# Performance work log

Measured on AMD Instinct MI355X. Metric: run time of the kernel, lower is better.

## Reference

```python
import jax, jax.numpy as jnp
import numpy as np

# int64 needed: hash primes (2654435761) exceed int32 range, matching torch int64 math
jax.config.update("jax_enable_x64", True)

T = 524288          # hash table size
F = 2               # features per entry
D = 3               # spatial dim
RES_MIN, RES_MAX, L, LAYER = 16.0, 512.0, 16, 8
GROWTH = np.exp((np.log(RES_MAX) - np.log(RES_MIN)) / (L - 1))
RES = float(GROWTH ** LAYER * RES_MIN)
PRIMES = jnp.array([1, 2654435761, 805459861], dtype=jnp.int64)
N_POINTS = 2097152  # I*R*M

# corner c uses ceil on dim d iff bit (D-1-d) of c is set, matching the torch corner ordering
_CORNER_MASK = ((jnp.arange(8)[:, None] >> (2 - jnp.arange(3)[None, :])) & 1).astype(bool)  # (8,3)


def setup_inputs() -> dict:
    key = jax.random.key(0)
    k1, k2 = jax.random.split(key)
    X = jax.random.uniform(k1, (N_POINTS, D), dtype=jnp.float32)
    hash_table = jax.random.normal(k2, (T, F), dtype=jnp.float32) * 1e-4
    return {"X": X, "hash_table": hash_table}


def reference(X, hash_table):
    Xs = X * (RES - 1.0)                      # (N,3)
    fl = jnp.floor(Xs)
    ce = jnp.ceil(Xs)
    fli = fl.astype(jnp.int64)
    cei = ce.astype(jnp.int64)
    # (N,8,3) cube corner integer coords
    cube = jnp.where(_CORNER_MASK[None], cei[:, None, :], fli[:, None, :])
    hm = cube * PRIMES                        # (N,8,3)
    idx = jnp.remainder(hm[..., 0] ^ hm[..., 1] ^ hm[..., 2], T)  # (N,8)
    vals = hash_table[idx]                    # (N,8,F) gather
    # trilinear interpolation, corner ordering as in the torch code
    w = Xs - fl                               # (N,3)
    w0, w1, w2 = w[:, 0:1], w[:, 1:2], w[:, 2:3]
    p00 = vals[:, 0] * (1 - w0) + vals[:, 4] * w0
    p01 = vals[:, 1] * (1 - w0) + vals[:, 5] * w0
    p10 = vals[:, 2] * (1 - w0) + vals[:, 6] * w0
    p11 = vals[:, 3] * (1 - w0) + vals[:, 7] * w0
    p0 = p00 * (1 - w1) + p10 * w1
    p1 = p01 * (1 - w1) + p11 * w1
    return p0 * (1 - w2) + p1 * w2            # (N,F)
```

## Files before the change

kernel.cpp:

```cpp
#include <hip/hip_runtime.h>
#include <math.h>


#define HT_SIZE 524288u
#define HT_MASK (HT_SIZE - 1u)
#define PRIME_Y 2654435761u
#define PRIME_Z 805459861u
#define N_POINTS 2097152

__global__ __launch_bounds__(256) void hashgrid_interp_kernel(
    const float* __restrict__ X,
    const float* __restrict__ table,
    float2* __restrict__ out,
    float scale)
{
    int i = blockIdx.x * blockDim.x + threadIdx.x;
    if (i >= N_POINTS) return;

    float xs = X[3 * i + 0] * scale;
    float ys = X[3 * i + 1] * scale;
    float zs = X[3 * i + 2] * scale;

    float fx = floorf(xs), fy = floorf(ys), fz = floorf(zs);
    float wx = xs - fx,   wy = ys - fy,   wz = zs - fz;

    unsigned ix0 = (unsigned)(int)fx;
    unsigned iy0 = (unsigned)(int)fy;
    unsigned iz0 = (unsigned)(int)fz;
    unsigned ix1 = (unsigned)(int)ceilf(xs);
    unsigned iy1 = (unsigned)(int)ceilf(ys);
    unsigned iz1 = (unsigned)(int)ceilf(zs);

    unsigned hx0 = ix0;
    unsigned hx1 = ix1;
    unsigned hy0 = iy0 * PRIME_Y;
    unsigned hy1 = iy1 * PRIME_Y;
    unsigned hz0 = iz0 * PRIME_Z;
    unsigned hz1 = iz1 * PRIME_Z;

    const float2* tb = (const float2*)table;

    float2 v0 = tb[(hx0 ^ hy0 ^ hz0) & HT_MASK];
    float2 v1 = tb[(hx0 ^ hy0 ^ hz1) & HT_MASK];
    float2 v2 = tb[(hx0 ^ hy1 ^ hz0) & HT_MASK];
    float2 v3 = tb[(hx0 ^ hy1 ^ hz1) & HT_MASK];
    float2 v4 = tb[(hx1 ^ hy0 ^ hz0) & HT_MASK];
    float2 v5 = tb[(hx1 ^ hy0 ^ hz1) & HT_MASK];
    float2 v6 = tb[(hx1 ^ hy1 ^ hz0) & HT_MASK];
    float2 v7 = tb[(hx1 ^ hy1 ^ hz1) & HT_MASK];

    float omx = 1.0f - wx, omy = 1.0f - wy, omz = 1.0f - wz;

    float p00x = v0.x * omx + v4.x * wx;
    float p00y = v0.y * omx + v4.y * wx;
    float p01x = v1.x * omx + v5.x * wx;
    float p01y = v1.y * omx + v5.y * wx;
    float p10x = v2.x * omx + v6.x * wx;
    float p10y = v2.y * omx + v6.y * wx;
    float p11x = v3.x * omx + v7.x * wx;
    float p11y = v3.y * omx + v7.y * wx;

    float p0x = p00x * omy + p10x * wy;
    float p0y = p00y * omy + p10y * wy;
    float p1x = p01x * omy + p11x * wy;
    float p1y = p01y * omy + p11y * wy;

    float2 r;
    r.x = p0x * omz + p1x * wz;
    r.y = p0y * omz + p1y * wz;
    out[i] = r;
}

extern "C" void kernel_launch(void* const* d_in, const int* in_sizes, int n_in,
                              void* d_out, int out_size, void* d_ws, size_t ws_size,
                              hipStream_t stream) {
    const float* X     = (const float*)d_in[0];
    const float* table = (const float*)d_in[1];
    float2* out = (float2*)d_out;

    double growth = exp((log(512.0) - log(16.0)) / 15.0);
    double res = pow(growth, 8.0) * 16.0;
    float scale = (float)(res - 1.0);

    int block = 256;
    int grid = (N_POINTS + block - 1) / block;
    hashgrid_interp_kernel<<<grid, block, 0, stream>>>(X, table, out, scale);
}
```

Before: 61.91 us.

## Process four points per thread with vectorized nontemporal loads and stores

Each thread now handles four points: it reads their 12 coordinates as three 16-byte nontemporal loads, computes all 32 hash indices, issues all 32 gathers together, and writes results as two 16-byte nontemporal stores. This targets the strided 4-byte coordinate loads and is meant to expose more memory-level parallelism per thread for the random table gathers. It launches a quarter as many threads and uses more registers per thread, which may lower occupancy. The bounds check is gone, relying on N being an exact multiple of the block size times four.

```diff
diff --git a/kernel.cpp b/kernel.cpp
--- a/kernel.cpp
+++ b/kernel.cpp
@@ -2,87 +2,109 @@
 #include <math.h>
 
 
-#define HT_SIZE 524288u
-#define HT_MASK (HT_SIZE - 1u)
-#define PRIME_Y 2654435761u
-#define PRIME_Z 805459861u
+#define HT_MASK  524287u
+#define PRIME_Y  2654435761u
+#define PRIME_Z  805459861u
 #define N_POINTS 2097152
+#define PPT      4
+
+typedef float vfloat4 __attribute__((ext_vector_type(4)));
 
 __global__ __launch_bounds__(256) void hashgrid_interp_kernel(
-    const float* __restrict__ X,
-    const float* __restrict__ table,
-    float2* __restrict__ out,
+    const vfloat4* __restrict__ X4,
+    const float2* __restrict__ tb,
+    vfloat4* __restrict__ out4,
     float scale)
 {
-    int i = blockIdx.x * blockDim.x + threadIdx.x;
-    if (i >= N_POINTS) return;
+    int t = blockIdx.x * blockDim.x + threadIdx.x;
 
-    float xs = X[3 * i + 0] * scale;
-    float ys = X[3 * i + 1] * scale;
-    float zs = X[3 * i + 2] * scale;
+    vfloat4 q0 = __builtin_nontemporal_load(&X4[3 * t + 0]);
+    vfloat4 q1 = __builtin_nontemporal_load(&X4[3 * t + 1]);
+    vfloat4 q2 = __builtin_nontemporal_load(&X4[3 * t + 2]);
 
-    float fx = floorf(xs), fy = floorf(ys), fz = floorf(zs);
-    float wx = xs - fx,   wy = ys - fy,   wz = zs - fz;
+    float px[PPT] = {q0.x, q0.w, q1.z, q2.y};
+    float py[PPT] = {q0.y, q1.x, q1.w, q2.z};
+    float pz[PPT] = {q0.z, q1.y, q2.x, q2.w};
 
-    unsigned ix0 = (unsigned)(int)fx;
-    unsigned iy0 = (unsigned)(int)fy;
-    unsigned iz0 = (unsigned)(int)fz;
-    unsigned ix1 = (unsigned)(int)ceilf(xs);
-    unsigned iy1 = (unsigned)(int)ceilf(ys);
-    unsigned iz1 = (unsigned)(int)ceilf(zs);
+    unsigned idx[PPT][8];
+    float wx[PPT], wy[PPT], wz[PPT];
 
-    unsigned hx0 = ix0;
-    unsigned hx1 = ix1;
-    unsigned hy0 = iy0 * PRIME_Y;
-    unsigned hy1 = iy1 * PRIME_Y;
-    unsigned hz0 = iz0 * PRIME_Z;
-    unsigned hz1 = iz1 * PRIME_Z;
+    #pragma unroll
+    for (int p = 0; p < PPT; ++p) {
+        float xs = px[p] * scale;
+        float ys = py[p] * scale;
+        float zs = pz[p] * scale;
 
-    const float2* tb = (const float2*)table;
+        float fx = floorf(xs), fy = floorf(ys), fz = floorf(zs);
+        wx[p] = xs - fx;  wy[p] = ys - fy;  wz[p] = zs - fz;
 
-    float2 v0 = tb[(hx0 ^ hy0 ^ hz0) & HT_MASK];
-    float2 v1 = tb[(hx0 ^ hy0 ^ hz1) & HT_MASK];
-    float2 v2 = tb[(hx0 ^ hy1 ^ hz0) & HT_MASK];
-    float2 v3 = tb[(hx0 ^ hy1 ^ hz1) & HT_MASK];
-    float2 v4 = tb[(hx1 ^ hy0 ^ hz0) & HT_MASK];
-    float2 v5 = tb[(hx1 ^ hy0 ^ hz1) & HT_MASK];
-    float2 v6 = tb[(hx1 ^ hy1 ^ hz0) & HT_MASK];
-    float2 v7 = tb[(hx1 ^ hy1 ^ hz1) & HT_MASK];
+        unsigned hx0 = (unsigned)(int)fx;
+        unsigned hy0 = (unsigned)(int)fy * PRIME_Y;
+        unsigned hz0 = (unsigned)(int)fz * PRIME_Z;
+        unsigned hx1 = (unsigned)(int)ceilf(xs);
+        unsigned hy1 = (unsigned)(int)ceilf(ys) * PRIME_Y;
+        unsigned hz1 = (unsigned)(int)ceilf(zs) * PRIME_Z;
 
-    float omx = 1.0f - wx, omy = 1.0f - wy, omz = 1.0f - wz;
+        idx[p][0] = (hx0 ^ hy0 ^ hz0) & HT_MASK;
+        idx[p][1] = (hx0 ^ hy0 ^ hz1) & HT_MASK;
+        idx[p][2] = (hx0 ^ hy1 ^ hz0) & HT_MASK;
+        idx[p][3] = (hx0 ^ hy1 ^ hz1) & HT_MASK;
+        idx[p][4] = (hx1 ^ hy0 ^ hz0) & HT_MASK;
+        idx[p][5] = (hx1 ^ hy0 ^ hz1) & HT_MASK;
+        idx[p][6] = (hx1 ^ hy1 ^ hz0) & HT_MASK;
+        idx[p][7] = (hx1 ^ hy1 ^ hz1) & HT_MASK;
+    }
 
-    float p00x = v0.x * omx + v4.x * wx;
-    float p00y = v0.y * omx + v4.y * wx;
-    float p01x = v1.x * omx + v5.x * wx;
-    float p01y = v1.y * omx + v5.y * wx;
-    float p10x = v2.x * omx + v6.x * wx;
-    float p10y = v2.y * omx + v6.y * wx;
-    float p11x = v3.x * omx + v7.x * wx;
-    float p11y = v3.y * omx + v7.y * wx;
+    float2 v[PPT][8];
+    #pragma unroll
+    for (int p = 0; p < PPT; ++p) {
+        #pragma unroll
+        for (int c = 0; c < 8; ++c) {
+            v[p][c] = tb[idx[p][c]];
+        }
+    }
 
-    float p0x = p00x * omy + p10x * wy;
-    float p0y = p00y * omy + p10y * wy;
-    float p1x = p01x * omy + p11x * wy;
-    float p1y = p01y * omy + p11y * wy;
+    float2 r[PPT];
+    #pragma unroll
+    for (int p = 0; p < PPT; ++p) {
+        float omx = 1.0f - wx[p], omy = 1.0f - wy[p], omz = 1.0f - wz[p];
 
-    float2 r;
-    r.x = p0x * omz + p1x * wz;
-    r.y = p0y * omz + p1y * wz;
-    out[i] = r;
+        float p00x = v[p][0].x * omx + v[p][4].x * wx[p];
+        float p00y = v[p][0].y * omx + v[p][4].y * wx[p];
+        float p01x = v[p][1].x * omx + v[p][5].x * wx[p];
+        float p01y = v[p][1].y * omx + v[p][5].y * wx[p];
+        float p10x = v[p][2].x * omx + v[p][6].x * wx[p];
+        float p10y = v[p][2].y * omx + v[p][6].y * wx[p];
+        float p11x = v[p][3].x * omx + v[p][7].x * wx[p];
+        float p11y = v[p][3].y * omx + v[p][7].y * wx[p];
+
+        float p0x = p00x * omy + p10x * wy[p];
+        float p0y = p00y * omy + p10y * wy[p];
+        float p1x = p01x * omy + p11x * wy[p];
+        float p1y = p01y * omy + p11y * wy[p];
+
+        r[p].x = p0x * omz + p1x * wz[p];
+        r[p].y = p0y * omz + p1y * wz[p];
+    }
+
+    vfloat4 o0 = {r[0].x, r[0].y, r[1].x, r[1].y};
+    vfloat4 o1 = {r[2].x, r[2].y, r[3].x, r[3].y};
+    __builtin_nontemporal_store(o0, &out4[2 * t + 0]);
+    __builtin_nontemporal_store(o1, &out4[2 * t + 1]);
 }
 
 extern "C" void kernel_launch(void* const* d_in, const int* in_sizes, int n_in,
                               void* d_out, int out_size, void* d_ws, size_t ws_size,
                               hipStream_t stream) {
-    const float* X     = (const float*)d_in[0];
-    const float* table = (const float*)d_in[1];
-    float2* out = (float2*)d_out;
+    const vfloat4* X4   = (const vfloat4*)d_in[0];
+    const float2* table = (const float2*)d_in[1];
+    vfloat4* out4 = (vfloat4*)d_out;
 
     double growth = exp((log(512.0) - log(16.0)) / 15.0);
     double res = pow(growth, 8.0) * 16.0;
     float scale = (float)(res - 1.0);
 
     int block = 256;
-    int grid = (N_POINTS + block - 1) / block;
-    hashgrid_interp_kernel<<<grid, block, 0, stream>>>(X, table, out, scale);
+    int grid = N_POINTS / (block * PPT);
+    hashgrid_interp_kernel<<<grid, block, 0, stream>>>(X4, table, out4, scale);
 }
```

After: 64.40 us. 4.0% more time.
